# Kernel tuning notes

Measured on AMD Instinct MI355X. Metric: run time of the kernel, lower is better.

The kernel has to match this reference:

```python
import jax, jax.numpy as jnp
import numpy as np

S = 8192          # total tokens (8 images x 1024 patches)
DIM = 1280        # hidden_size
H = 16            # num_heads
DH = DIM // H     # head_dim = 80
N_SEG = 8         # number of image segments (equal-length)


def setup_inputs() -> dict:
    key = jax.random.key(0)
    ks = jax.random.split(key, 8)
    hidden_states = jax.random.normal(ks[0], (S, DIM), dtype=jnp.float32)
    ang = jax.random.uniform(ks[1], (S, DH), dtype=jnp.float32) * (2.0 * np.pi)
    cos = jnp.cos(ang)
    sin = jnp.sin(ang)
    cu_seqlens = (jnp.arange(N_SEG + 1, dtype=jnp.int32) * (S // N_SEG))
    qkv_w = jax.random.normal(ks[2], (3 * DIM, DIM), dtype=jnp.float32) * 0.02
    qkv_b = jax.random.normal(ks[3], (3 * DIM,), dtype=jnp.float32) * 0.02
    proj_w = jax.random.normal(ks[4], (DIM, DIM), dtype=jnp.float32) * 0.02
    proj_b = jax.random.normal(ks[5], (DIM,), dtype=jnp.float32) * 0.02
    return {
        "hidden_states": hidden_states,
        "cos": cos,
        "sin": sin,
        "qkv_w": qkv_w,
        "qkv_b": qkv_b,
        "proj_w": proj_w,
        "proj_b": proj_b,
        "cu_seqlens": cu_seqlens,
    }


def _rotate_half(x):
    d = x.shape[-1] // 2
    return jnp.concatenate([-x[..., d:], x[..., :d]], axis=-1)


def reference(hidden_states, cos, sin, qkv_w, qkv_b, proj_w, proj_b, cu_seqlens):
    s, dim = hidden_states.shape
    dh = cos.shape[-1]
    h = dim // dh
    n_seg = cu_seqlens.shape[0] - 1  # static; segments are equal-length
    L = s // n_seg
    scale = dh ** -0.5

    # fused QKV projection: [S, 3, H, DH]
    qkv = (hidden_states @ qkv_w.T + qkv_b).reshape(s, 3, h, dh)
    q, k, v = qkv[:, 0], qkv[:, 1], qkv[:, 2]

    # RoPE (fp32, broadcast cos/sin over heads)
    cos_b = cos[:, None, :].astype(jnp.float32)
    sin_b = sin[:, None, :].astype(jnp.float32)
    qf, kf = q.astype(jnp.float32), k.astype(jnp.float32)
    q = (qf * cos_b + _rotate_half(qf) * sin_b).astype(q.dtype)
    k = (kf * cos_b + _rotate_half(kf) * sin_b).astype(k.dtype)

    # per-segment (block-diagonal) attention: reshape to [n_seg, L, H, DH]
    qs = q.reshape(n_seg, L, h, dh)
    ks = k.reshape(n_seg, L, h, dh)
    vs = v.reshape(n_seg, L, h, dh)
    scores = jnp.einsum("glhd,gmhd->ghlm", qs, ks) * scale
    attn = jax.nn.softmax(scores, axis=-1)
    out = jnp.einsum("ghlm,gmhd->glhd", attn, vs).reshape(s, dim)
    return out @ proj_w.T + proj_b
```

## Files before the change

### kernel.cpp

```cpp
#include <hip/hip_runtime.h>
#include <stdint.h>

typedef unsigned short u16;
typedef unsigned int u32;
typedef __attribute__((ext_vector_type(8))) short short8;
typedef __attribute__((ext_vector_type(4))) float f32x4;

#define DEV __device__ __forceinline__

constexpr int S = 8192;
constexpr int DIM = 1280;
constexpr int H = 16;
constexpr int DH = 80;
constexpr int LSEG = 1024;
constexpr int QKVN = 3 * DIM;
constexpr float SCALE = 0.11180339887498949f;

DEV u16 f2bf(float f) {
  u32 u = __float_as_uint(f);
  return (u16)((u + 0x7FFFu + ((u >> 16) & 1u)) >> 16);
}
DEV float bf2f(u16 h) { return __uint_as_float(((u32)h) << 16); }

DEV void glds16(const void* g, void* l) {
  __builtin_amdgcn_global_load_lds((__attribute__((address_space(1))) void*)g,
                                   (__attribute__((address_space(3))) void*)l,
                                   16, 0, 0);
}
DEV f32x4 mfma16(short8 a, short8 b, f32x4 c) {
  return __builtin_amdgcn_mfma_f32_16x16x32_bf16(a, b, c, 0, 0, 0);
}

__global__ __launch_bounds__(256) void cvt_kernel(
    const float* __restrict__ X, const float* __restrict__ Wq,
    const float* __restrict__ Wp, u16* __restrict__ Xb,
    u16* __restrict__ Wqb, u16* __restrict__ Wpb) {
  size_t i = ((size_t)blockIdx.x * 256 + threadIdx.x) * 4;
  const size_t n1 = (size_t)S * DIM;
  const size_t n2 = (size_t)QKVN * DIM;
  const size_t n3 = (size_t)DIM * DIM;
  const float* src; u16* dst; size_t off;
  if (i < n1)                { src = X;  dst = Xb;  off = i; }
  else if (i < n1 + n2)      { src = Wq; dst = Wqb; off = i - n1; }
  else if (i < n1 + n2 + n3) { src = Wp; dst = Wpb; off = i - n1 - n2; }
  else return;
  float4 v = *(const float4*)(src + off);
  ushort4 r;
  r.x = f2bf(v.x); r.y = f2bf(v.y); r.z = f2bf(v.z); r.w = f2bf(v.w);
  *(ushort4*)(dst + off) = r;
}

__global__ __launch_bounds__(256) void rope_kernel(
    const u16* __restrict__ QKV, const float* __restrict__ cosp,
    const float* __restrict__ sinp, u16* __restrict__ Qp, u16* __restrict__ Kp) {
  int idx = blockIdx.x * 256 + threadIdx.x;
  int s = idx / (H * 48);
  int rem = idx % (H * 48);
  int h = rem / 48, td = rem % 48;
  size_t pbase = (size_t)(s * 16 + h) * 96;
  if (td < 40) {
    float c0 = cosp[s * DH + td], c1 = cosp[s * DH + td + 40];
    float s0 = sinp[s * DH + td], s1 = sinp[s * DH + td + 40];
    size_t base = (size_t)s * QKVN + h * DH + td;
    float q0 = bf2f(QKV[base]), q1 = bf2f(QKV[base + 40]);
    Qp[pbase + td]      = f2bf((q0 * c0 - q1 * s0) * SCALE);
    Qp[pbase + td + 40] = f2bf((q1 * c1 + q0 * s1) * SCALE);
    float k0 = bf2f(QKV[base + DIM]), k1 = bf2f(QKV[base + DIM + 40]);
    Kp[pbase + td]      = f2bf(k0 * c0 - k1 * s0);
    Kp[pbase + td + 40] = f2bf(k1 * c1 + k0 * s1);
  } else {
    int j = td - 40;
    Qp[pbase + 80 + j] = 0; Qp[pbase + 88 + j] = 0;
    Kp[pbase + 80 + j] = 0; Kp[pbase + 88 + j] = 0;
  }
}

__global__ __launch_bounds__(256) void vtrans_kernel(
    const u16* __restrict__ QKV, u16* __restrict__ Vt) {
  __shared__ u16 Ls[64 * 88];
  const int s0 = blockIdx.x * 64, h = blockIdx.y;
  const int tid = threadIdx.x;
  for (int cc = tid; cc < 640; cc += 256) {
    int row = cc / 10, c = cc % 10;
    short8 v = *(const short8*)&QKV[(size_t)(s0 + row) * QKVN + 2 * DIM + h * 80 + c * 8];
    *(short8*)&Ls[row * 88 + c * 8] = v;
  }
  __syncthreads();
  for (int cc = tid; cc < 640; cc += 256) {
    int d = cc / 8, sc = cc % 8;
    u16 tmp[8];
#pragma unroll
    for (int j = 0; j < 8; j++) tmp[j] = Ls[(sc * 8 + j) * 88 + d];
    *(short8*)&Vt[(size_t)(h * 80 + d) * S + s0 + sc * 8] = *(short8*)tmp;
  }
}

template <bool OUT_F32>
__global__ __launch_bounds__(256, 2) void gemm_bt(
    const u16* __restrict__ A, const u16* __restrict__ B,
    const float* __restrict__ bias, void* __restrict__ C, int K, int N) {
  __shared__ u16 As[2][128 * 32];
  __shared__ u16 Bs[2][128 * 32];
  const int bid = blockIdx.x;
  const int xcd = bid & 7, j = bid >> 3;
  const int m0 = (xcd * 8 + (j & 7)) * 128;
  const int n0 = (j >> 3) * 128;
  const int tid = threadIdx.x;
  const int w = tid >> 6, lane = tid & 63;
  const int quad = lane >> 4, l16 = lane & 15;
  const int wr = (w >> 1) * 64, wc = (w & 1) * 64;
  const int lrow = lane >> 2;
  const int lcol = ((lane & 3) ^ (lrow & 3)) * 8;
  const u16* ga[4]; const u16* gb[4]; u16* la[4]; u16* lb[4];
#pragma unroll
  for (int i = 0; i < 4; i++) {
    int jj = w + 4 * i;
    int s = jj >> 3, c = jj & 7;
    ga[i] = A + (size_t)(m0 + c * 16 + lrow) * K + s * 32 + lcol;
    la[i] = &As[s][c * 512];
    gb[i] = B + (size_t)(n0 + c * 16 + lrow) * K + s * 32 + lcol;
    lb[i] = &Bs[s][c * 512];
  }
  const int fco = (quad ^ (l16 & 3)) * 8;
  f32x4 acc[4][4] = {};
  for (int k0 = 0; k0 < K; k0 += 64) {
    __syncthreads();
#pragma unroll
    for (int i = 0; i < 4; i++) { glds16(ga[i], la[i]); ga[i] += 64; }
#pragma unroll
    for (int i = 0; i < 4; i++) { glds16(gb[i], lb[i]); gb[i] += 64; }
    __syncthreads();
#pragma unroll
    for (int s = 0; s < 2; s++) {
      short8 af[4], bf[4];
#pragma unroll
      for (int i = 0; i < 4; i++)
        af[i] = *(const short8*)&As[s][(wr + i * 16 + l16) * 32 + fco];
#pragma unroll
      for (int i = 0; i < 4; i++)
        bf[i] = *(const short8*)&Bs[s][(wc + i * 16 + l16) * 32 + fco];
#pragma unroll
      for (int i = 0; i < 4; i++)
#pragma unroll
        for (int jj = 0; jj < 4; jj++)
          acc[i][jj] = mfma16(af[i], bf[jj], acc[i][jj]);
    }
  }
#pragma unroll
  for (int jj = 0; jj < 4; jj++) {
    int col = n0 + wc + jj * 16 + l16;
    float bv = bias[col];
#pragma unroll
    for (int i = 0; i < 4; i++) {
#pragma unroll
      for (int r = 0; r < 4; r++) {
        int row = m0 + wr + i * 16 + quad * 4 + r;
        float v = acc[i][jj][r] + bv;
        if (OUT_F32) ((float*)C)[(size_t)row * N + col] = v;
        else         ((u16*)C)[(size_t)row * N + col] = f2bf(v);
      }
    }
  }
}

__global__ __launch_bounds__(256, 2) void attn_kernel(
    const u16* __restrict__ Qp, const u16* __restrict__ Kp,
    const u16* __restrict__ Vt, u16* __restrict__ O) {
  __shared__ u16 Ks[128 * 104];
  __shared__ u16 Vs[83 * 136];
  __shared__ u16 Ps[8][16 * 72];
  const int bid = blockIdx.x;
  const int phi = bid & 7, qt = (bid >> 3) & 7, pj = bid >> 6;
  const int p = pj * 8 + phi;
  const int g = p >> 4, h = p & 15;
  const int tid = threadIdx.x;
  const int w = tid >> 6, lane = tid & 63;
  const int quad = lane >> 4, l16 = lane & 15;

  short8 aq[2][3];
  const size_t qbase = ((size_t)(g * LSEG + qt * 128 + w * 32 + l16)) * 1536 + h * 96;
#pragma unroll
  for (int mt = 0; mt < 2; mt++)
#pragma unroll
    for (int ks = 0; ks < 3; ks++)
      aq[mt][ks] = *(const short8*)&Qp[qbase + (size_t)mt * 16 * 1536 + ks * 32 + quad * 8];

  const u16* gp[12]; u16* lp[12]; int stp[12];
#pragma unroll
  for (int i = 0; i < 12; i++) {
    int c = w + 4 * i;
    if (c < 26) {
      int idx = c * 64 + lane;
      int key = idx / 13, rc = idx % 13;
      int col = rc * 8; if (col >= 96) col = 0;
      gp[i] = Kp + (size_t)(g * LSEG + key) * 1536 + h * 96 + col;
      stp[i] = 128 * 1536;
      lp[i] = &Ks[c * 512];
    } else {
      int cv = c - 26;
      int idx = cv * 64 + lane;
      int d = idx / 17, rc = idx % 17;
      int col = rc * 8; if (col >= 128) col = 0;
      if (d >= 80) d = 0;
      gp[i] = Vt + (size_t)(h * 80 + d) * S + g * LSEG + col;
      stp[i] = 128;
      lp[i] = &Vs[cv * 512];
    }
  }

  f32x4 o[2][5] = {};
  float lr[2][4] = {};

  for (int kb = 0; kb < LSEG / 128; kb++) {
    __syncthreads();
#pragma unroll
    for (int i = 0; i < 12; i++) { glds16(gp[i], lp[i]); gp[i] += stp[i]; }
    __syncthreads();
    f32x4 s[2][8] = {};
#pragma unroll
    for (int ks = 0; ks < 3; ks++) {
      short8 bk[8];
#pragma unroll
      for (int nt = 0; nt < 8; nt++)
        bk[nt] = *(const short8*)&Ks[(nt * 16 + l16) * 104 + ks * 32 + quad * 8];
#pragma unroll
      for (int mt = 0; mt < 2; mt++)
#pragma unroll
        for (int nt = 0; nt < 8; nt++)
          s[mt][nt] = mfma16(aq[mt][ks], bk[nt], s[mt][nt]);
    }
#pragma unroll
    for (int half = 0; half < 2; half++) {
      short8 vb[5][2];
#pragma unroll
      for (int t = 0; t < 5; t++)
#pragma unroll
        for (int u = 0; u < 2; u++)
          vb[t][u] = *(const short8*)&Vs[(t * 16 + l16) * 136 + half * 64 + u * 32 + quad * 8];
#pragma unroll
      for (int mt = 0; mt < 2; mt++) {
        u16* psw = &Ps[w * 2 + mt][0];
        const int nb = half * 4;
#pragma unroll
        for (int r = 0; r < 4; r++) {
          float p0 = __expf(s[mt][nb + 0][r]), p1 = __expf(s[mt][nb + 1][r]);
          float p2 = __expf(s[mt][nb + 2][r]), p3 = __expf(s[mt][nb + 3][r]);
          lr[mt][r] += (p0 + p1) + (p2 + p3);
          int row = quad * 4 + r;
          psw[row * 72 + l16]      = f2bf(p0);
          psw[row * 72 + 16 + l16] = f2bf(p1);
          psw[row * 72 + 32 + l16] = f2bf(p2);
          psw[row * 72 + 48 + l16] = f2bf(p3);
        }
        short8 pa0 = *(const short8*)&psw[l16 * 72 + quad * 8];
        short8 pa1 = *(const short8*)&psw[l16 * 72 + 32 + quad * 8];
#pragma unroll
        for (int t = 0; t < 5; t++)
          o[mt][t] = mfma16(pa0, vb[t][0], o[mt][t]);
#pragma unroll
        for (int t = 0; t < 5; t++)
          o[mt][t] = mfma16(pa1, vb[t][1], o[mt][t]);
      }
    }
  }
#pragma unroll
  for (int mt = 0; mt < 2; mt++)
#pragma unroll
    for (int r = 0; r < 4; r++) {
      float t = lr[mt][r];
#pragma unroll
      for (int off = 8; off >= 1; off >>= 1) t += __shfl_xor(t, off, 16);
      float inv = 1.f / t;
      int srow = g * LSEG + qt * 128 + w * 32 + mt * 16 + quad * 4 + r;
#pragma unroll
      for (int tt = 0; tt < 5; tt++)
        O[(size_t)srow * DIM + h * DH + tt * 16 + l16] = f2bf(o[mt][tt][r] * inv);
    }
}

extern "C" void kernel_launch(void* const* d_in, const int* in_sizes, int n_in,
                              void* d_out, int out_size, void* d_ws, size_t ws_size,
                              hipStream_t stream) {
  const float* X     = (const float*)d_in[0];
  const float* cosp  = (const float*)d_in[1];
  const float* sinp  = (const float*)d_in[2];
  const float* qkvw  = (const float*)d_in[3];
  const float* qkvb  = (const float*)d_in[4];
  const float* projw = (const float*)d_in[5];
  const float* projb = (const float*)d_in[6];
  float* out = (float*)d_out;

  u16* Xb   = (u16*)d_ws;
  u16* Wqb  = Xb   + (size_t)S * DIM;
  u16* Wpb  = Wqb  + (size_t)QKVN * DIM;
  u16* QKVb = Wpb  + (size_t)DIM * DIM;
  u16* Kp   = QKVb + (size_t)S * QKVN;
  u16* Vt   = Kp   + (size_t)S * H * 96;
  u16* Qp   = Xb;
  u16* AOb  = QKVb;

  cvt_kernel<<<16640, 256, 0, stream>>>(X, qkvw, projw, Xb, Wqb, Wpb);
  gemm_bt<false><<<30 * 64, 256, 0, stream>>>(Xb, Wqb, qkvb, QKVb, DIM, QKVN);
  rope_kernel<<<(S * H * 48) / 256, 256, 0, stream>>>(QKVb, cosp, sinp, Qp, Kp);
  vtrans_kernel<<<dim3(S / 64, H), 256, 0, stream>>>(QKVb, Vt);
  attn_kernel<<<1024, 256, 0, stream>>>(Qp, Kp, Vt, AOb);
  gemm_bt<true><<<10 * 64, 256, 0, stream>>>(AOb, Wpb, projb, out, DIM, DIM);
}
```

Baseline: 359.7 us.

## Double-buffer attention K/V tiles, use exp2, pack P stores, vectorize RoPE

The attention kernel moves from single-buffered 128-key tiles to double-buffered 64-key tiles, so the next tile's global-to-LDS load is issued while the current tile is computed, and one barrier per iteration is removed. Softmax uses exp2 with log2(e) folded into the Q scale, and probabilities are written to LDS as packed bf16 pairs through a key permutation. The V transpose is reordered to match that permutation. RoPE is rewritten to process 8 elements per thread with vector loads and stores. The main risks are the P/V permutation staying consistent and the extra LDS and loop overhead from smaller tiles.

```diff
diff --git a/kernel.cpp b/kernel.cpp
--- a/kernel.cpp
+++ b/kernel.cpp
@@ -1,4 +1,5 @@
 #include <hip/hip_runtime.h>
+#include <hip/hip_bf16.h>
 #include <stdint.h>
 
 typedef unsigned short u16;
@@ -14,13 +15,17 @@
 constexpr int DH = 80;
 constexpr int LSEG = 1024;
 constexpr int QKVN = 3 * DIM;
-constexpr float SCALE = 0.11180339887498949f;
+constexpr float SCALE = 0.11180339887498949f * 1.4426950408889634f;
 
 DEV u16 f2bf(float f) {
   u32 u = __float_as_uint(f);
   return (u16)((u + 0x7FFFu + ((u >> 16) & 1u)) >> 16);
 }
 DEV float bf2f(u16 h) { return __uint_as_float(((u32)h) << 16); }
+DEV u32 pkbf(float a, float b) {
+  __hip_bfloat162 t = __float22bfloat162_rn(float2{a, b});
+  u32 r; __builtin_memcpy(&r, &t, 4); return r;
+}
 
 DEV void glds16(const void* g, void* l) {
   __builtin_amdgcn_global_load_lds((__attribute__((address_space(1))) void*)g,
@@ -54,24 +59,45 @@
     const u16* __restrict__ QKV, const float* __restrict__ cosp,
     const float* __restrict__ sinp, u16* __restrict__ Qp, u16* __restrict__ Kp) {
   int idx = blockIdx.x * 256 + threadIdx.x;
-  int s = idx / (H * 48);
-  int rem = idx % (H * 48);
-  int h = rem / 48, td = rem % 48;
-  size_t pbase = (size_t)(s * 16 + h) * 96;
-  if (td < 40) {
-    float c0 = cosp[s * DH + td], c1 = cosp[s * DH + td + 40];
-    float s0 = sinp[s * DH + td], s1 = sinp[s * DH + td + 40];
-    size_t base = (size_t)s * QKVN + h * DH + td;
-    float q0 = bf2f(QKV[base]), q1 = bf2f(QKV[base + 40]);
-    Qp[pbase + td]      = f2bf((q0 * c0 - q1 * s0) * SCALE);
-    Qp[pbase + td + 40] = f2bf((q1 * c1 + q0 * s1) * SCALE);
-    float k0 = bf2f(QKV[base + DIM]), k1 = bf2f(QKV[base + DIM + 40]);
-    Kp[pbase + td]      = f2bf(k0 * c0 - k1 * s0);
-    Kp[pbase + td + 40] = f2bf(k1 * c1 + k0 * s1);
-  } else {
-    int j = td - 40;
-    Qp[pbase + 80 + j] = 0; Qp[pbase + 88 + j] = 0;
-    Kp[pbase + 80 + j] = 0; Kp[pbase + 88 + j] = 0;
+  int c = idx % 5;
+  int sh = idx / 5;
+  int s = sh >> 4, h = sh & 15;
+  const size_t gbase = (size_t)s * QKVN + h * DH + c * 8;
+  const size_t pbase = (size_t)sh * 96 + c * 8;
+  short8 q0 = *(const short8*)&QKV[gbase];
+  short8 q1 = *(const short8*)&QKV[gbase + 40];
+  short8 k0 = *(const short8*)&QKV[gbase + DIM];
+  short8 k1 = *(const short8*)&QKV[gbase + DIM + 40];
+  float4 ca0 = *(const float4*)&cosp[s * DH + c * 8];
+  float4 ca1 = *(const float4*)&cosp[s * DH + c * 8 + 4];
+  float4 cb0 = *(const float4*)&cosp[s * DH + c * 8 + 40];
+  float4 cb1 = *(const float4*)&cosp[s * DH + c * 8 + 44];
+  float4 sa0 = *(const float4*)&sinp[s * DH + c * 8];
+  float4 sa1 = *(const float4*)&sinp[s * DH + c * 8 + 4];
+  float4 sb0 = *(const float4*)&sinp[s * DH + c * 8 + 40];
+  float4 sb1 = *(const float4*)&sinp[s * DH + c * 8 + 44];
+  float ca[8] = {ca0.x, ca0.y, ca0.z, ca0.w, ca1.x, ca1.y, ca1.z, ca1.w};
+  float cb[8] = {cb0.x, cb0.y, cb0.z, cb0.w, cb1.x, cb1.y, cb1.z, cb1.w};
+  float sa[8] = {sa0.x, sa0.y, sa0.z, sa0.w, sa1.x, sa1.y, sa1.z, sa1.w};
+  float sb[8] = {sb0.x, sb0.y, sb0.z, sb0.w, sb1.x, sb1.y, sb1.z, sb1.w};
+  short8 qo0, qo1, ko0, ko1;
+#pragma unroll
+  for (int j = 0; j < 8; j++) {
+    float qa = bf2f((u16)q0[j]), qb = bf2f((u16)q1[j]);
+    float ka = bf2f((u16)k0[j]), kb = bf2f((u16)k1[j]);
+    qo0[j] = (short)f2bf((qa * ca[j] - qb * sa[j]) * SCALE);
+    qo1[j] = (short)f2bf((qb * cb[j] + qa * sb[j]) * SCALE);
+    ko0[j] = (short)f2bf(ka * ca[j] - kb * sa[j]);
+    ko1[j] = (short)f2bf(kb * cb[j] + ka * sb[j]);
+  }
+  *(short8*)&Qp[pbase]      = qo0;
+  *(short8*)&Qp[pbase + 40] = qo1;
+  *(short8*)&Kp[pbase]      = ko0;
+  *(short8*)&Kp[pbase + 40] = ko1;
+  if (c == 0) {
+    short8 z = {};
+    *(short8*)&Qp[pbase + 80] = z; *(short8*)&Qp[pbase + 88] = z;
+    *(short8*)&Kp[pbase + 80] = z; *(short8*)&Kp[pbase + 88] = z;
   }
 }
 
@@ -90,7 +116,11 @@
     int d = cc / 8, sc = cc % 8;
     u16 tmp[8];
 #pragma unroll
-    for (int j = 0; j < 8; j++) tmp[j] = Ls[(sc * 8 + j) * 88 + d];
+    for (int j = 0; j < 8; j++) {
+      int op = sc * 8 + j;
+      int key = ((op & 3) << 4) + (op >> 2);
+      tmp[j] = Ls[key * 88 + d];
+    }
     *(short8*)&Vt[(size_t)(h * 80 + d) * S + s0 + sc * 8] = *(short8*)tmp;
   }
 }
@@ -166,9 +196,9 @@
 __global__ __launch_bounds__(256, 2) void attn_kernel(
     const u16* __restrict__ Qp, const u16* __restrict__ Kp,
     const u16* __restrict__ Vt, u16* __restrict__ O) {
-  __shared__ u16 Ks[128 * 104];
-  __shared__ u16 Vs[83 * 136];
-  __shared__ u16 Ps[8][16 * 72];
+  __shared__ u16 Ks[2][64 * 104];
+  __shared__ u16 Vs[2][86 * 72];
+  __shared__ u16 Ps[4][16 * 72];
   const int bid = blockIdx.x;
   const int phi = bid & 7, qt = (bid >> 3) & 7, pj = bid >> 6;
   const int p = pj * 8 + phi;
@@ -185,82 +215,92 @@
     for (int ks = 0; ks < 3; ks++)
       aq[mt][ks] = *(const short8*)&Qp[qbase + (size_t)mt * 16 * 1536 + ks * 32 + quad * 8];
 
-  const u16* gp[12]; u16* lp[12]; int stp[12];
-#pragma unroll
-  for (int i = 0; i < 12; i++) {
+  const u16* gp[7]; u16* lp0[7]; u16* lp1[7]; int stp[7]; bool act[7];
+#pragma unroll
+  for (int i = 0; i < 7; i++) {
     int c = w + 4 * i;
-    if (c < 26) {
-      int idx = c * 64 + lane;
+    act[i] = (c < 25);
+    int cc = act[i] ? c : 0;
+    if (cc < 13) {
+      int idx = cc * 64 + lane;
       int key = idx / 13, rc = idx % 13;
       int col = rc * 8; if (col >= 96) col = 0;
       gp[i] = Kp + (size_t)(g * LSEG + key) * 1536 + h * 96 + col;
-      stp[i] = 128 * 1536;
-      lp[i] = &Ks[c * 512];
+      stp[i] = 64 * 1536;
+      lp0[i] = &Ks[0][cc * 512]; lp1[i] = &Ks[1][cc * 512];
     } else {
-      int cv = c - 26;
+      int cv = cc - 13;
       int idx = cv * 64 + lane;
-      int d = idx / 17, rc = idx % 17;
-      int col = rc * 8; if (col >= 128) col = 0;
+      int d = idx / 9, rc = idx % 9;
+      int col = rc * 8; if (col >= 64) col = 0;
       if (d >= 80) d = 0;
       gp[i] = Vt + (size_t)(h * 80 + d) * S + g * LSEG + col;
-      stp[i] = 128;
-      lp[i] = &Vs[cv * 512];
-    }
-  }
+      stp[i] = 64;
+      lp0[i] = &Vs[0][cv * 512]; lp1[i] = &Vs[1][cv * 512];
+    }
+  }
+#pragma unroll
+  for (int i = 0; i < 7; i++)
+    if (act[i]) { glds16(gp[i], lp0[i]); gp[i] += stp[i]; }
 
   f32x4 o[2][5] = {};
   float lr[2][4] = {};
-
-  for (int kb = 0; kb < LSEG / 128; kb++) {
+  u16* psw = &Ps[w][0];
+
+  for (int kb = 0; kb < LSEG / 64; kb++) {
+    const int b = kb & 1;
     __syncthreads();
-#pragma unroll
-    for (int i = 0; i < 12; i++) { glds16(gp[i], lp[i]); gp[i] += stp[i]; }
-    __syncthreads();
-    f32x4 s[2][8] = {};
+    if (kb < LSEG / 64 - 1) {
+      if (b == 0) {
+#pragma unroll
+        for (int i = 0; i < 7; i++)
+          if (act[i]) { glds16(gp[i], lp1[i]); gp[i] += stp[i]; }
+      } else {
+#pragma unroll
+        for (int i = 0; i < 7; i++)
+          if (act[i]) { glds16(gp[i], lp0[i]); gp[i] += stp[i]; }
+      }
+    }
+    f32x4 s[2][4] = {};
 #pragma unroll
     for (int ks = 0; ks < 3; ks++) {
-      short8 bk[8];
-#pragma unroll
-      for (int nt = 0; nt < 8; nt++)
-        bk[nt] = *(const short8*)&Ks[(nt * 16 + l16) * 104 + ks * 32 + quad * 8];
+      short8 bk[4];
+#pragma unroll
+      for (int nt = 0; nt < 4; nt++)
+        bk[nt] = *(const short8*)&Ks[b][(nt * 16 + l16) * 104 + ks * 32 + quad * 8];
 #pragma unroll
       for (int mt = 0; mt < 2; mt++)
 #pragma unroll
-        for (int nt = 0; nt < 8; nt++)
+        for (int nt = 0; nt < 4; nt++)
           s[mt][nt] = mfma16(aq[mt][ks], bk[nt], s[mt][nt]);
     }
-#pragma unroll
-    for (int half = 0; half < 2; half++) {
-      short8 vb[5][2];
+    short8 vb[5][2];
+#pragma unroll
+    for (int t = 0; t < 5; t++)
+#pragma unroll
+      for (int u = 0; u < 2; u++)
+        vb[t][u] = *(const short8*)&Vs[b][(t * 16 + l16) * 72 + u * 32 + quad * 8];
+#pragma unroll
+    for (int mt = 0; mt < 2; mt++) {
+#pragma unroll
+      for (int r = 0; r < 4; r++) {
+        float p0 = __builtin_amdgcn_exp2f(s[mt][0][r]);
+        float p1 = __builtin_amdgcn_exp2f(s[mt][1][r]);
+        float p2 = __builtin_amdgcn_exp2f(s[mt][2][r]);
+        float p3 = __builtin_amdgcn_exp2f(s[mt][3][r]);
+        lr[mt][r] += (p0 + p1) + (p2 + p3);
+        int row = quad * 4 + r;
+        uint2 pk; pk.x = pkbf(p0, p1); pk.y = pkbf(p2, p3);
+        *(uint2*)&psw[row * 72 + l16 * 4] = pk;
+      }
+      short8 pa0 = *(const short8*)&psw[l16 * 72 + quad * 8];
+      short8 pa1 = *(const short8*)&psw[l16 * 72 + 32 + quad * 8];
 #pragma unroll
       for (int t = 0; t < 5; t++)
-#pragma unroll
-        for (int u = 0; u < 2; u++)
-          vb[t][u] = *(const short8*)&Vs[(t * 16 + l16) * 136 + half * 64 + u * 32 + quad * 8];
-#pragma unroll
-      for (int mt = 0; mt < 2; mt++) {
-        u16* psw = &Ps[w * 2 + mt][0];
-        const int nb = half * 4;
-#pragma unroll
-        for (int r = 0; r < 4; r++) {
-          float p0 = __expf(s[mt][nb + 0][r]), p1 = __expf(s[mt][nb + 1][r]);
-          float p2 = __expf(s[mt][nb + 2][r]), p3 = __expf(s[mt][nb + 3][r]);
-          lr[mt][r] += (p0 + p1) + (p2 + p3);
-          int row = quad * 4 + r;
-          psw[row * 72 + l16]      = f2bf(p0);
-          psw[row * 72 + 16 + l16] = f2bf(p1);
-          psw[row * 72 + 32 + l16] = f2bf(p2);
-          psw[row * 72 + 48 + l16] = f2bf(p3);
-        }
-        short8 pa0 = *(const short8*)&psw[l16 * 72 + quad * 8];
-        short8 pa1 = *(const short8*)&psw[l16 * 72 + 32 + quad * 8];
-#pragma unroll
-        for (int t = 0; t < 5; t++)
-          o[mt][t] = mfma16(pa0, vb[t][0], o[mt][t]);
-#pragma unroll
-        for (int t = 0; t < 5; t++)
-          o[mt][t] = mfma16(pa1, vb[t][1], o[mt][t]);
-      }
+        o[mt][t] = mfma16(pa0, vb[t][0], o[mt][t]);
+#pragma unroll
+      for (int t = 0; t < 5; t++)
+        o[mt][t] = mfma16(pa1, vb[t][1], o[mt][t]);
     }
   }
 #pragma unroll
@@ -301,7 +341,7 @@
 
   cvt_kernel<<<16640, 256, 0, stream>>>(X, qkvw, projw, Xb, Wqb, Wpb);
   gemm_bt<false><<<30 * 64, 256, 0, stream>>>(Xb, Wqb, qkvb, QKVb, DIM, QKVN);
-  rope_kernel<<<(S * H * 48) / 256, 256, 0, stream>>>(QKVb, cosp, sinp, Qp, Kp);
+  rope_kernel<<<(S * H * 5) / 256, 256, 0, stream>>>(QKVb, cosp, sinp, Qp, Kp);
   vtrans_kernel<<<dim3(S / 64, H), 256, 0, stream>>>(QKVb, Vt);
   attn_kernel<<<1024, 256, 0, stream>>>(Qp, Kp, Vt, AOb);
   gemm_bt<true><<<10 * 64, 256, 0, stream>>>(AOb, Wpb, projb, out, DIM, DIM);
```

New measurement: 342.0 us. -4.9%, faster.
